# Performance work log

Measured on AMD Instinct MI355X. Metric: run time of the kernel, lower is better.

Reference implementation:

```python
import jax, jax.numpy as jnp
import numpy as np

B, T, C = 4, 2048, 1024
H, D = 16, 64


def setup_inputs() -> dict:
    key = jax.random.key(0)
    ks = jax.random.split(key, 5)
    x = jax.random.normal(ks[0], (B, T, C), dtype=jnp.float32)
    Wq = jax.random.normal(ks[1], (H, C, D), dtype=jnp.float32) * (C ** -0.5)
    Wk = jax.random.normal(ks[2], (H, C, D), dtype=jnp.float32) * (C ** -0.5)
    Wv = jax.random.normal(ks[3], (H, C, D), dtype=jnp.float32) * (C ** -0.5)
    Wp = jax.random.normal(ks[4], (H * D, C), dtype=jnp.float32) * ((H * D) ** -0.5)
    bp = jnp.zeros((C,), dtype=jnp.float32)
    return {"x": x, "Wq": Wq, "Wk": Wk, "Wv": Wv, "Wp": Wp, "bp": bp}


def reference(x, Wq, Wk, Wv, Wp, bp):
    # per-head projections (bias-free): [B,H,T,D]
    q = jnp.einsum('btc,hcd->bhtd', x, Wq)
    k = jnp.einsum('btc,hcd->bhtd', x, Wk)
    v = jnp.einsum('btc,hcd->bhtd', x, Wv)
    # NOTE: source multiplies by sqrt(head_size) (faithful to original code)
    scale = jnp.asarray(D ** 0.5, x.dtype)
    att = jnp.einsum('bhtd,bhsd->bhts', q, k) * scale  # [B,H,T,T]
    causal = jnp.tril(jnp.ones((T, T), dtype=bool))
    att = jnp.where(causal, att, jnp.asarray(-jnp.inf, att.dtype))
    att = jax.nn.softmax(att, axis=-1)
    out = jnp.einsum('bhts,bhsd->bhtd', att, v)  # [B,H,T,D]
    out = out.transpose(0, 2, 1, 3).reshape(B, T, H * D)  # head concat
    return out @ Wp + bp
```

## Files before the change

kernel.cpp:

```cpp
#include <hip/hip_runtime.h>

#define B_ 4
#define T_ 2048
#define C_ 1024
#define H_ 16
#define D_ 64

typedef _Float16 f16x8 __attribute__((ext_vector_type(8)));
typedef __fp16 fp16x2 __attribute__((ext_vector_type(2)));
typedef float f32x4 __attribute__((ext_vector_type(4)));
typedef unsigned short u16x8 __attribute__((ext_vector_type(8)));

#define MFMA16 __builtin_amdgcn_mfma_f32_16x16x32_f16
#define SCALE2 11.541560327111707f

__device__ __forceinline__ unsigned pk2(float a, float b) {
    fp16x2 p = __builtin_amdgcn_cvt_pkrtz(a, b);
    return __builtin_bit_cast(unsigned, p);
}

__device__ __forceinline__ void gl_lds16(const _Float16* g, unsigned short* lds) {
    __builtin_amdgcn_global_load_lds(
        (const __attribute__((address_space(1))) unsigned int*)g,
        (__attribute__((address_space(3))) unsigned int*)lds, 16, 0, 0);
}

__global__ __launch_bounds__(256) void convx_kernel(const float* __restrict__ x,
                                                    _Float16* __restrict__ Xf) {
    size_t i = ((size_t)blockIdx.x * 256 + threadIdx.x) * 8;
    f32x4 a = *reinterpret_cast<const f32x4*>(x + i);
    f32x4 b = *reinterpret_cast<const f32x4*>(x + i + 4);
    f16x8 o;
    o[0] = (_Float16)a[0]; o[1] = (_Float16)a[1]; o[2] = (_Float16)a[2]; o[3] = (_Float16)a[3];
    o[4] = (_Float16)b[0]; o[5] = (_Float16)b[1]; o[6] = (_Float16)b[2]; o[7] = (_Float16)b[3];
    *reinterpret_cast<f16x8*>(Xf + i) = o;
}

__global__ __launch_bounds__(256) void convw_qkv_kernel(
    const float* __restrict__ Wq, const float* __restrict__ Wk, const float* __restrict__ Wv,
    _Float16* __restrict__ Wqt, _Float16* __restrict__ Wkt, _Float16* __restrict__ Wvt)
{
    __shared__ unsigned short Wl[128][72];
    const int ct = blockIdx.x, h = blockIdx.y, m = blockIdx.z;
    const float* src = (m == 0 ? Wq : (m == 1 ? Wk : Wv)) + ((size_t)h * C_ + ct * 128) * D_;
    _Float16* dst = (m == 0 ? Wqt : (m == 1 ? Wkt : Wvt));
    const int tid = threadIdx.x;
    {
        int r = tid >> 1, half = tid & 1;
        #pragma unroll
        for (int i = 0; i < 8; i++) {
            f32x4 v = *reinterpret_cast<const f32x4*>(src + (size_t)r * D_ + half * 32 + i * 4);
            #pragma unroll
            for (int j = 0; j < 4; j++)
                Wl[r][half * 32 + i * 4 + j] = __builtin_bit_cast(unsigned short, (_Float16)v[j]);
        }
    }
    __syncthreads();
    {
        int d = tid >> 2, seg = tid & 3;
        #pragma unroll
        for (int i = 0; i < 4; i++) {
            u16x8 o;
            #pragma unroll
            for (int j = 0; j < 8; j++) o[j] = Wl[seg * 32 + i * 8 + j][d];
            *reinterpret_cast<u16x8*>((unsigned short*)dst + ((size_t)h * D_ + d) * C_ + ct * 128 + seg * 32 + i * 8) = o;
        }
    }
}

__global__ __launch_bounds__(256) void convw_p_kernel(const float* __restrict__ Wp,
                                                      _Float16* __restrict__ Wpt)
{
    __shared__ unsigned short Pl[64][72];
    const int jt = blockIdx.x, kt = blockIdx.y;
    const int tid = threadIdx.x;
    {
        int r = tid >> 2, seg = tid & 3;
        #pragma unroll
        for (int i = 0; i < 4; i++) {
            f32x4 v = *reinterpret_cast<const f32x4*>(Wp + (size_t)(kt * 64 + r) * C_ + jt * 64 + seg * 16 + i * 4);
            #pragma unroll
            for (int j = 0; j < 4; j++)
                Pl[r][seg * 16 + i * 4 + j] = __builtin_bit_cast(unsigned short, (_Float16)v[j]);
        }
    }
    __syncthreads();
    {
        int jj = tid >> 2, kseg = tid & 3;
        #pragma unroll
        for (int i = 0; i < 2; i++) {
            u16x8 o;
            #pragma unroll
            for (int j = 0; j < 8; j++) o[j] = Pl[kseg * 16 + i * 8 + j][jj];
            *reinterpret_cast<u16x8*>((unsigned short*)Wpt + (size_t)(jt * 64 + jj) * C_ + kt * 64 + kseg * 16 + i * 8) = o;
        }
    }
}

__global__ __launch_bounds__(256) void qkv4_kernel(
    const _Float16* __restrict__ Xf, const _Float16* __restrict__ Wcat,
    _Float16* __restrict__ Qf, _Float16* __restrict__ Kf, _Float16* __restrict__ Vt)
{
    __shared__ unsigned short As[128 * 64];
    __shared__ unsigned short Bs[192 * 64];
    const int rt = blockIdx.x, ct = blockIdx.y;
    const int row0 = rt * 128, n0 = ct * 192;
    const int tid = threadIdx.x, wid = tid >> 6, lane = tid & 63;
    const int l15 = lane & 15, g = lane >> 4;
    const int wr = wid >> 1, wc = wid & 1;
    const int lrow = lane >> 3, lcol = (lane & 7) * 8;

    f32x4 acc[4][6];
    #pragma unroll
    for (int mi = 0; mi < 4; mi++)
        #pragma unroll
        for (int ni = 0; ni < 6; ni++) { f32x4 z = {0.f,0.f,0.f,0.f}; acc[mi][ni] = z; }

    for (int k0 = 0; k0 < C_; k0 += 64) {
        __syncthreads();
        #pragma unroll
        for (int i = 0; i < 4; i++) {
            int c = wid * 4 + i;
            gl_lds16(Xf + (size_t)(row0 + c * 8 + lrow) * C_ + k0 + lcol, &As[c * 512]);
        }
        #pragma unroll
        for (int i = 0; i < 6; i++) {
            int c = wid * 6 + i;
            gl_lds16(Wcat + (size_t)(n0 + c * 8 + lrow) * C_ + k0 + lcol, &Bs[c * 512]);
        }
        __syncthreads();
        #pragma unroll
        for (int kk = 0; kk < 2; kk++) {
            f16x8 af[4];
            #pragma unroll
            for (int mi = 0; mi < 4; mi++)
                af[mi] = *reinterpret_cast<const f16x8*>(&As[(wr * 64 + mi * 16 + l15) * 64 + kk * 32 + g * 8]);
            #pragma unroll
            for (int ni = 0; ni < 6; ni++) {
                f16x8 bf = *reinterpret_cast<const f16x8*>(&Bs[(wc * 96 + ni * 16 + l15) * 64 + kk * 32 + g * 8]);
                #pragma unroll
                for (int mi = 0; mi < 4; mi++)
                    acc[mi][ni] = MFMA16(af[mi], bf, acc[mi][ni], 0, 0, 0);
            }
        }
    }

    const int b = row0 >> 11;
    const int t0b = (row0 & (T_ - 1)) + wr * 64;
    #pragma unroll
    for (int ni = 0; ni < 6; ni++) {
        const int n = n0 + wc * 96 + ni * 16;
        const int region = n >> 10;
        const int h = (n >> 6) & 15;
        const int d0 = n & 63;
        if (region < 2) {
            _Float16* dst = region ? Kf : Qf;
            const float osc = region ? 1.0f : SCALE2;
            const size_t hb = ((size_t)(b * H_ + h)) * T_ * D_;
            #pragma unroll
            for (int mi = 0; mi < 4; mi++)
                #pragma unroll
                for (int r = 0; r < 4; r++) {
                    int t = t0b + mi * 16 + g * 4 + r;
                    dst[hb + (size_t)t * D_ + d0 + l15] = (_Float16)(acc[mi][ni][r] * osc);
                }
        } else {
            const size_t vbase = ((size_t)(b * H_ + h)) * D_ * T_;
            const int d = d0 + l15;
            #pragma unroll
            for (int mi = 0; mi < 4; mi++) {
                int t = t0b + mi * 16 + g * 4;
                uint2 w;
                w.x = pk2(acc[mi][ni][0], acc[mi][ni][1]);
                w.y = pk2(acc[mi][ni][2], acc[mi][ni][3]);
                *reinterpret_cast<uint2*>((unsigned short*)Vt + vbase + (size_t)d * T_ + t) = w;
            }
        }
    }
}

__global__ __launch_bounds__(256) void flash_kernel(
    const _Float16* __restrict__ Qf, const _Float16* __restrict__ Kf,
    const _Float16* __restrict__ Vt, _Float16* __restrict__ att)
{
    __shared__ __align__(16) unsigned short Ks[2][128 * 64];
    __shared__ __align__(16) unsigned short Vs[2][64 * 128];
    __shared__ __align__(16) unsigned short Ps[4][32 * 32];
    const int bh = blockIdx.x;
    const int p = (int)blockIdx.y;
    const int bb = bh >> 4, h = bh & 15;
    const int tid = threadIdx.x, wid = tid >> 6, lane = tid & 63;
    const int l15 = lane & 15, g = lane >> 4;

    const _Float16* Qb = Qf + (size_t)bh * T_ * D_;
    const _Float16* Kb = Kf + (size_t)bh * T_ * D_;
    const _Float16* Vb = Vt + (size_t)bh * D_ * T_;

    const int srow = lane >> 3;
    const int sunit = (lane & 7) ^ srow;
    const int r0k = wid * 32;
    const int vsrow = lane >> 4;
    const int r0v = wid * 16;

    char* const pbase = (char*)&Ps[wid][0];

    f16x8 ones;
    #pragma unroll
    for (int j = 0; j < 8; j++) ones[j] = (_Float16)1.0f;

    for (int pass = 0; pass < 2; pass++) {
        const int qt = pass ? p : (15 - p);
        const int q0 = qt * 128;
        const int qw = q0 + wid * 32;

        f16x8 qf[2][2];
        #pragma unroll
        for (int mt = 0; mt < 2; mt++)
            #pragma unroll
            for (int kk = 0; kk < 2; kk++)
                qf[mt][kk] = *reinterpret_cast<const f16x8*>(Qb + (size_t)(qw + mt * 16 + l15) * D_ + kk * 32 + g * 8);

        f32x4 accO[4][2];
        #pragma unroll
        for (int nt = 0; nt < 4; nt++)
            #pragma unroll
            for (int mt = 0; mt < 2; mt++) { f32x4 z = {0.f,0.f,0.f,0.f}; accO[nt][mt] = z; }
        float m[2] = { -1e30f, -1e30f };
        float l[2] = { 0.f, 0.f };

        const int nSup = qt + 1;
        const int mySub = (qw + 95) >> 6;

        #pragma unroll
        for (int i = 0; i < 4; i++) {
            int krow = r0k + i * 8 + srow;
            gl_lds16(Kb + (size_t)krow * D_ + sunit * 8, &Ks[0][(r0k + i * 8) * 64]);
            int vrow = r0v + i * 4 + vsrow;
            int vsunit = (lane & 15) ^ (vrow & 7);
            gl_lds16(Vb + (size_t)vrow * T_ + vsunit * 8, &Vs[0][(r0v + i * 4) * 128]);
        }
        __syncthreads();

#define SUB_TILE(SP, SH, MASKED)                                                    \
    {                                                                               \
        const int kv0 = ((SP) * 2 + (SH)) * 64;                                     \
        f32x4 s[4][2];                                                              \
        _Pragma("unroll")                                                           \
        for (int st = 0; st < 4; st++)                                              \
            _Pragma("unroll")                                                       \
            for (int mt = 0; mt < 2; mt++) { f32x4 z = {0.f,0.f,0.f,0.f}; s[st][mt] = z; } \
        _Pragma("unroll")                                                           \
        for (int kk = 0; kk < 2; kk++) {                                            \
            f16x8 kfr[4];                                                           \
            _Pragma("unroll")                                                       \
            for (int st = 0; st < 4; st++) {                                        \
                int row = (SH) * 64 + st * 16 + l15;                                \
                kfr[st] = *reinterpret_cast<const f16x8*>(                          \
                    kb128 + row * 128 + (((kk * 4 + g) ^ (row & 7)) * 16));         \
            }                                                                       \
            _Pragma("unroll")                                                       \
            for (int st = 0; st < 4; st++)                                          \
                _Pragma("unroll")                                                   \
                for (int mt = 0; mt < 2; mt++)                                      \
                    s[st][mt] = MFMA16(kfr[st], qf[mt][kk], s[st][mt], 0, 0, 0);    \
        }                                                                           \
        unsigned pw[2][4][2];                                                       \
        _Pragma("unroll")                                                           \
        for (int mt = 0; mt < 2; mt++) {                                            \
            if (MASKED) {                                                           \
                const int qrow = qw + mt * 16 + l15;                                \
                _Pragma("unroll")                                                   \
                for (int st = 0; st < 4; st++)                                      \
                    _Pragma("unroll")                                               \
                    for (int rr = 0; rr < 4; rr++) {                                \
                        int kv = kv0 + st * 16 + g * 4 + rr;                        \
                        s[st][mt][rr] = (kv <= qrow) ? s[st][mt][rr] : -1e30f;      \
                    }                                                               \
            }                                                                       \
            float vmax = -1e30f;                                                    \
            _Pragma("unroll")                                                       \
            for (int st = 0; st < 4; st++)                                          \
                _Pragma("unroll")                                                   \
                for (int rr = 0; rr < 4; rr++)                                      \
                    vmax = fmaxf(vmax, s[st][mt][rr]);                              \
            vmax = fmaxf(vmax, __shfl_xor(vmax, 16, 64));                           \
            vmax = fmaxf(vmax, __shfl_xor(vmax, 32, 64));                           \
            if (__any(vmax > m[mt])) {                                              \
                float mnew = fmaxf(m[mt], vmax);                                    \
                float alpha = __builtin_amdgcn_exp2f(m[mt] - mnew);                 \
                m[mt] = mnew;                                                       \
                l[mt] *= alpha;                                                     \
                _Pragma("unroll")                                                   \
                for (int nt = 0; nt < 4; nt++) accO[nt][mt] *= alpha;               \
            }                                                                       \
            _Pragma("unroll")                                                       \
            for (int st = 0; st < 4; st++) {                                        \
                float p0 = __builtin_amdgcn_exp2f(s[st][mt][0] - m[mt]);            \
                float p1 = __builtin_amdgcn_exp2f(s[st][mt][1] - m[mt]);            \
                float p2 = __builtin_amdgcn_exp2f(s[st][mt][2] - m[mt]);            \
                float p3 = __builtin_amdgcn_exp2f(s[st][mt][3] - m[mt]);            \
                pw[mt][st][0] = pk2(p0, p1);                                        \
                pw[mt][st][1] = pk2(p2, p3);                                        \
            }                                                                       \
        }                                                                           \
        f32x4 rsacc[2];                                                             \
        { f32x4 z = {0.f,0.f,0.f,0.f}; rsacc[0] = z; rsacc[1] = z; }                \
        _Pragma("unroll")                                                           \
        for (int ph = 0; ph < 2; ph++) {                                            \
            _Pragma("unroll")                                                       \
            for (int mt = 0; mt < 2; mt++) {                                        \
                const int r = mt * 16 + l15;                                        \
                const int swz = ((r >> 1) & 3) << 4;                                \
                char* prow = pbase + r * 64;                                        \
                _Pragma("unroll")                                                   \
                for (int stl = 0; stl < 2; stl++) {                                 \
                    uint2 w;                                                        \
                    w.x = pw[mt][ph * 2 + stl][0];                                  \
                    w.y = pw[mt][ph * 2 + stl][1];                                  \
                    *reinterpret_cast<uint2*>(prow + ((stl * 32 + g * 8) ^ swz)) = w; \
                }                                                                   \
            }                                                                       \
            f16x8 pb[2];                                                            \
            _Pragma("unroll")                                                       \
            for (int mt = 0; mt < 2; mt++) {                                        \
                const int r = mt * 16 + l15;                                        \
                const int swz = ((r >> 1) & 3) << 4;                                \
                pb[mt] = *reinterpret_cast<const f16x8*>(pbase + r * 64 + ((g * 16) ^ swz)); \
            }                                                                       \
            rsacc[0] = MFMA16(ones, pb[0], rsacc[0], 0, 0, 0);                      \
            rsacc[1] = MFMA16(ones, pb[1], rsacc[1], 0, 0, 0);                      \
            _Pragma("unroll")                                                       \
            for (int nt = 0; nt < 4; nt++) {                                        \
                int row = nt * 16 + l15;                                            \
                int unit = ((SH) * 8 + ph * 4 + g) ^ (row & 7);                     \
                f16x8 vf = *reinterpret_cast<const f16x8*>(                         \
                    vb128 + row * 256 + unit * 16);                                 \
                _Pragma("unroll")                                                   \
                for (int mt = 0; mt < 2; mt++)                                      \
                    accO[nt][mt] = MFMA16(vf, pb[mt], accO[nt][mt], 0, 0, 0);       \
            }                                                                       \
        }                                                                           \
        l[0] += rsacc[0][0];                                                        \
        l[1] += rsacc[1][0];                                                        \
    }

#define SUPER_BODY(SP, BUF)                                                         \
    {                                                                               \
        if ((SP) + 1 < nSup) {                                                      \
            const int kvn = ((SP) + 1) * 128;                                       \
            _Pragma("unroll")                                                       \
            for (int i = 0; i < 4; i++) {                                           \
                int krow = r0k + i * 8 + srow;                                      \
                gl_lds16(Kb + (size_t)(kvn + krow) * D_ + sunit * 8,                \
                         &Ks[(BUF) ^ 1][(r0k + i * 8) * 64]);                       \
                int vrow = r0v + i * 4 + vsrow;                                     \
                int vsunit = (lane & 15) ^ (vrow & 7);                              \
                gl_lds16(Vb + (size_t)vrow * T_ + kvn + vsunit * 8,                 \
                         &Vs[(BUF) ^ 1][(r0v + i * 4) * 128]);                      \
            }                                                                       \
        }                                                                           \
        const char* kb128 = (const char*)&Ks[BUF][0];                               \
        const char* vb128 = (const char*)&Vs[BUF][0];                               \
        if ((SP) * 2 + 1 < mySub)      { SUB_TILE(SP, 0, 0) }                       \
        else if ((SP) * 2 < mySub)     { SUB_TILE(SP, 0, 1) }                       \
        if ((SP) * 2 + 2 < mySub)      { SUB_TILE(SP, 1, 0) }                       \
        else if ((SP) * 2 + 1 < mySub) { SUB_TILE(SP, 1, 1) }                       \
        __syncthreads();                                                            \
    }

        for (int sp = 0; sp < nSup; sp += 2) {
            SUPER_BODY(sp, 0)
            if (sp + 1 < nSup) {
                SUPER_BODY(sp + 1, 1)
            }
        }
#undef SUPER_BODY
#undef SUB_TILE

        #pragma unroll
        for (int mt = 0; mt < 2; mt++) {
            float inv = 1.0f / l[mt];
            int t = qw + mt * 16 + l15;
            #pragma unroll
            for (int nt = 0; nt < 4; nt++) {
                f32x4 o = accO[nt][mt] * inv;
                uint2 w;
                w.x = pk2(o[0], o[1]);
                w.y = pk2(o[2], o[3]);
                size_t off = ((size_t)(bb * T_ + t)) * (H_ * D_) + h * D_ + nt * 16 + g * 4;
                *reinterpret_cast<uint2*>((unsigned short*)att + off) = w;
            }
        }
    }
}

__global__ __launch_bounds__(256) void proj2_kernel(
    const _Float16* __restrict__ att, const _Float16* __restrict__ Wpt,
    const float* __restrict__ bp, float* __restrict__ out)
{
    __shared__ unsigned short As[128 * 64];
    __shared__ unsigned short Bs[128 * 64];
    const int rt = blockIdx.x, ct = blockIdx.y;
    const int row0 = rt * 128, n0 = ct * 128;
    const int tid = threadIdx.x, wid = tid >> 6, lane = tid & 63;
    const int l15 = lane & 15, g = lane >> 4;
    const int wr = wid >> 1, wc = wid & 1;
    const int lrow = lane >> 3, lcol = (lane & 7) * 8;

    f32x4 acc[4][4];
    #pragma unroll
    for (int mi = 0; mi < 4; mi++)
        #pragma unroll
        for (int ni = 0; ni < 4; ni++) { f32x4 z = {0.f,0.f,0.f,0.f}; acc[mi][ni] = z; }

    for (int k0 = 0; k0 < C_; k0 += 64) {
        __syncthreads();
        #pragma unroll
        for (int i = 0; i < 4; i++) {
            int c = wid * 4 + i;
            gl_lds16(att + (size_t)(row0 + c * 8 + lrow) * C_ + k0 + lcol, &As[c * 512]);
            gl_lds16(Wpt + (size_t)(n0   + c * 8 + lrow) * C_ + k0 + lcol, &Bs[c * 512]);
        }
        __syncthreads();
        #pragma unroll
        for (int kk = 0; kk < 2; kk++) {
            f16x8 af[4], bf[4];
            #pragma unroll
            for (int mi = 0; mi < 4; mi++)
                af[mi] = *reinterpret_cast<const f16x8*>(&As[(wr * 64 + mi * 16 + l15) * 64 + kk * 32 + g * 8]);
            #pragma unroll
            for (int ni = 0; ni < 4; ni++)
                bf[ni] = *reinterpret_cast<const f16x8*>(&Bs[(wc * 64 + ni * 16 + l15) * 64 + kk * 32 + g * 8]);
            #pragma unroll
            for (int mi = 0; mi < 4; mi++)
                #pragma unroll
                for (int ni = 0; ni < 4; ni++)
                    acc[mi][ni] = MFMA16(af[mi], bf[ni], acc[mi][ni], 0, 0, 0);
        }
    }

    #pragma unroll
    for (int mi = 0; mi < 4; mi++)
        #pragma unroll
        for (int ni = 0; ni < 4; ni++) {
            int col = n0 + wc * 64 + ni * 16 + l15;
            float bias = bp[col];
            #pragma unroll
            for (int r = 0; r < 4; r++) {
                int row = row0 + wr * 64 + mi * 16 + g * 4 + r;
                out[(size_t)row * C_ + col] = acc[mi][ni][r] + bias;
            }
        }
}

extern "C" void kernel_launch(void* const* d_in, const int* in_sizes, int n_in,
                              void* d_out, int out_size, void* d_ws, size_t ws_size,
                              hipStream_t stream) {
    const float* x  = (const float*)d_in[0];
    const float* Wq = (const float*)d_in[1];
    const float* Wk = (const float*)d_in[2];
    const float* Wv = (const float*)d_in[3];
    const float* Wp = (const float*)d_in[4];
    const float* bp = (const float*)d_in[5];
    float* out = (float*)d_out;

    _Float16* Xf  = (_Float16*)d_ws;
    _Float16* Wqt = Xf  + (size_t)8388608;
    _Float16* Wkt = Wqt + (size_t)1048576;
    _Float16* Wvt = Wkt + (size_t)1048576;
    _Float16* Wpt = Wvt + (size_t)1048576;
    _Float16* Qf  = Wpt + (size_t)1048576;
    _Float16* Kf  = Qf  + (size_t)8388608;
    _Float16* Vt  = Kf  + (size_t)8388608;
    _Float16* att = Vt  + (size_t)8388608;

    convx_kernel<<<4096, 256, 0, stream>>>(x, Xf);
    convw_qkv_kernel<<<dim3(8, 16, 3), 256, 0, stream>>>(Wq, Wk, Wv, Wqt, Wkt, Wvt);
    convw_p_kernel<<<dim3(16, 16), 256, 0, stream>>>(Wp, Wpt);
    qkv4_kernel<<<dim3(64, 16), 256, 0, stream>>>(Xf, Wqt, Qf, Kf, Vt);
    flash_kernel<<<dim3(64, 8), 256, 0, stream>>>(Qf, Kf, Vt, att);
    proj2_kernel<<<dim3(64, 8), 256, 0, stream>>>(att, Wpt, bp, out);
}
```

Baseline: 184.5 us.

## Double-buffer LDS in QKV GEMM to overlap global loads with MFMA

Splits the QKV projection's shared-memory tiles into two buffers and prefetches the next K-slice with global_load_lds while the current slice is consumed by MFMAs. Partial vmcnt waits and raw s_barrier replace the two full __syncthreads per iteration, and s_setprio raises wave priority during the MFMA section. The aim is to hide global-memory latency in the QKV GEMM. It doubles LDS use to 80 KB per block, which may lower occupancy.

```diff
diff --git a/kernel.cpp b/kernel.cpp
--- a/kernel.cpp
+++ b/kernel.cpp
@@ -97,12 +97,12 @@
     }
 }
 
-__global__ __launch_bounds__(256) void qkv4_kernel(
+__global__ __launch_bounds__(256) void qkv5_kernel(
     const _Float16* __restrict__ Xf, const _Float16* __restrict__ Wcat,
     _Float16* __restrict__ Qf, _Float16* __restrict__ Kf, _Float16* __restrict__ Vt)
 {
-    __shared__ unsigned short As[128 * 64];
-    __shared__ unsigned short Bs[192 * 64];
+    __shared__ unsigned short As[2][128 * 64];
+    __shared__ unsigned short Bs[2][192 * 64];
     const int rt = blockIdx.x, ct = blockIdx.y;
     const int row0 = rt * 128, n0 = ct * 192;
     const int tid = threadIdx.x, wid = tid >> 6, lane = tid & 63;
@@ -116,34 +116,59 @@
         #pragma unroll
         for (int ni = 0; ni < 6; ni++) { f32x4 z = {0.f,0.f,0.f,0.f}; acc[mi][ni] = z; }
 
-    for (int k0 = 0; k0 < C_; k0 += 64) {
-        __syncthreads();
-        #pragma unroll
-        for (int i = 0; i < 4; i++) {
-            int c = wid * 4 + i;
-            gl_lds16(Xf + (size_t)(row0 + c * 8 + lrow) * C_ + k0 + lcol, &As[c * 512]);
-        }
-        #pragma unroll
-        for (int i = 0; i < 6; i++) {
-            int c = wid * 6 + i;
-            gl_lds16(Wcat + (size_t)(n0 + c * 8 + lrow) * C_ + k0 + lcol, &Bs[c * 512]);
-        }
-        __syncthreads();
-        #pragma unroll
-        for (int kk = 0; kk < 2; kk++) {
-            f16x8 af[4];
-            #pragma unroll
-            for (int mi = 0; mi < 4; mi++)
-                af[mi] = *reinterpret_cast<const f16x8*>(&As[(wr * 64 + mi * 16 + l15) * 64 + kk * 32 + g * 8]);
-            #pragma unroll
-            for (int ni = 0; ni < 6; ni++) {
-                f16x8 bf = *reinterpret_cast<const f16x8*>(&Bs[(wc * 96 + ni * 16 + l15) * 64 + kk * 32 + g * 8]);
-                #pragma unroll
-                for (int mi = 0; mi < 4; mi++)
-                    acc[mi][ni] = MFMA16(af[mi], bf, acc[mi][ni], 0, 0, 0);
-            }
-        }
-    }
+#define STAGE(BUF, K0)                                                              \
+    {                                                                               \
+        _Pragma("unroll")                                                           \
+        for (int i = 0; i < 4; i++) {                                               \
+            int c = wid * 4 + i;                                                    \
+            gl_lds16(Xf + (size_t)(row0 + c * 8 + lrow) * C_ + (K0) + lcol,         \
+                     &As[BUF][c * 512]);                                            \
+        }                                                                           \
+        _Pragma("unroll")                                                           \
+        for (int i = 0; i < 6; i++) {                                               \
+            int c = wid * 6 + i;                                                    \
+            gl_lds16(Wcat + (size_t)(n0 + c * 8 + lrow) * C_ + (K0) + lcol,         \
+                     &Bs[BUF][c * 512]);                                            \
+        }                                                                           \
+    }
+
+#define KSTEP(T, BUF)                                                               \
+    {                                                                               \
+        if ((T) + 1 < 16) {                                                         \
+            STAGE((BUF) ^ 1, ((T) + 1) * 64)                                        \
+            asm volatile("s_waitcnt vmcnt(10)" ::: "memory");                       \
+        } else {                                                                    \
+            asm volatile("s_waitcnt vmcnt(0)" ::: "memory");                        \
+        }                                                                           \
+        __builtin_amdgcn_s_barrier();              \
+        __builtin_amdgcn_s_setprio(1);                                              \
+        _Pragma("unroll")                                                           \
+        for (int kk = 0; kk < 2; kk++) {                                            \
+            f16x8 af[4];                                                            \
+            _Pragma("unroll")                                                       \
+            for (int mi = 0; mi < 4; mi++)                                          \
+                af[mi] = *reinterpret_cast<const f16x8*>(                           \
+                    &As[BUF][(wr * 64 + mi * 16 + l15) * 64 + kk * 32 + g * 8]);    \
+            _Pragma("unroll")                                                       \
+            for (int ni = 0; ni < 6; ni++) {                                        \
+                f16x8 bf = *reinterpret_cast<const f16x8*>(                         \
+                    &Bs[BUF][(wc * 96 + ni * 16 + l15) * 64 + kk * 32 + g * 8]);    \
+                _Pragma("unroll")                                                   \
+                for (int mi = 0; mi < 4; mi++)                                      \
+                    acc[mi][ni] = MFMA16(af[mi], bf, acc[mi][ni], 0, 0, 0);         \
+            }                                                                       \
+        }                                                                           \
+        __builtin_amdgcn_s_setprio(0);                                              \
+        __builtin_amdgcn_s_barrier();                 \
+    }
+
+    STAGE(0, 0)
+    for (int t = 0; t < 16; t += 2) {
+        KSTEP(t, 0)
+        KSTEP(t + 1, 1)
+    }
+#undef KSTEP
+#undef STAGE
 
     const int b = row0 >> 11;
     const int t0b = (row0 & (T_ - 1)) + wr * 64;
@@ -477,7 +502,7 @@
     convx_kernel<<<4096, 256, 0, stream>>>(x, Xf);
     convw_qkv_kernel<<<dim3(8, 16, 3), 256, 0, stream>>>(Wq, Wk, Wv, Wqt, Wkt, Wvt);
     convw_p_kernel<<<dim3(16, 16), 256, 0, stream>>>(Wp, Wpt);
-    qkv4_kernel<<<dim3(64, 16), 256, 0, stream>>>(Xf, Wqt, Qf, Kf, Vt);
+    qkv5_kernel<<<dim3(64, 16), 256, 0, stream>>>(Xf, Wqt, Qf, Kf, Vt);
     flash_kernel<<<dim3(64, 8), 256, 0, stream>>>(Qf, Kf, Vt, att);
     proj2_kernel<<<dim3(64, 8), 256, 0, stream>>>(att, Wpt, bp, out);
 }
```

After: 223.0 us. 20.9% more time.
